# Optimization experiments

Measured on AMD Instinct MI355X. Metric: run time of the kernel, lower is better.

## Reference

```python
import jax, jax.numpy as jnp
import numpy as np

B, L, D = 2048, 64, 512


def setup_inputs() -> dict:
    key = jax.random.key(0)
    ks = jax.random.split(key, 20)
    s = 1.0 / np.sqrt(D)
    inp = {
        "query_entity_encoding": jax.random.normal(ks[0], (B, L, D), jnp.float32),
        "relation_encoding": jax.random.normal(ks[1], (B, D), jnp.float32),
        "mask_emb": jax.random.normal(ks[2], (1, D), jnp.float32),
        "pos_e": jax.random.normal(ks[3], (100, D), jnp.float32),
        "pos_r": jax.random.normal(ks[4], (100, D), jnp.float32),
        "We_q": jax.random.normal(ks[5], (D, D), jnp.float32) * s,
        "be_q": jnp.zeros((D,), jnp.float32),
        "We_k": jax.random.normal(ks[6], (D, D), jnp.float32) * s,
        "be_k": jnp.zeros((D,), jnp.float32),
        "We_v": jax.random.normal(ks[7], (D, D), jnp.float32) * s,
        "be_v": jnp.zeros((D,), jnp.float32),
        "Wr_q": jax.random.normal(ks[8], (D, D), jnp.float32) * s,
        "br_q": jnp.zeros((D,), jnp.float32),
        "Wr_k": jax.random.normal(ks[9], (D, D), jnp.float32) * s,
        "br_k": jnp.zeros((D,), jnp.float32),
        "Wr_v": jax.random.normal(ks[10], (D, D), jnp.float32) * s,
        "br_v": jnp.zeros((D,), jnp.float32),
    }
    return inp


def _linear(x, W, b):
    # torch nn.Linear: y = x @ W.T + b
    return jnp.einsum("bld,ed->ble", x, W) + b


def reference(query_entity_encoding, relation_encoding, mask_emb, pos_e, pos_r,
              We_q, be_q, We_k, be_k, We_v, be_v,
              Wr_q, br_q, Wr_k, br_k, Wr_v, br_v):
    b, l, d = query_entity_encoding.shape  # l <= 99 assumed (matches init spec)
    # append mask token, add positional encodings
    mask_tok = jnp.broadcast_to(mask_emb[None, :, :], (b, 1, d))
    ent = jnp.concatenate([query_entity_encoding, mask_tok], axis=1)  # [b, l+1, d]
    ent = ent + pos_e[: l + 1][None, :, :]
    rel = relation_encoding[:, None, :] + pos_r[:l][None, :, :]  # [b, l, d]
    # six projections
    Qe, Ke, Ve = _linear(ent, We_q, be_q), _linear(ent, We_k, be_k), _linear(ent, We_v, be_v)
    Qr, Kr, Vr = _linear(rel, Wr_q, br_q), _linear(rel, Wr_k, br_k), _linear(rel, Wr_v, br_v)
    # block-concat attention == attention over concatenated streams
    Q = jnp.concatenate([Qe, Qr], axis=1)  # [b, 2l+1, d]
    K = jnp.concatenate([Ke, Kr], axis=1)
    V = jnp.concatenate([Ve, Vr], axis=1)
    scale = 1.0 / jnp.sqrt(jnp.asarray(d, Q.dtype))
    A = jnp.einsum("bqd,bkd->bqk", Q, K) * scale
    A = jax.nn.softmax(A, axis=-1)
    out = jnp.einsum("bqk,bkd->bqd", A, V)
    return out[:, 0]
```

## Files before the change

kernel.cpp:

```cpp
#include <hip/hip_runtime.h>
#include <math.h>


using s16x8 = __attribute__((ext_vector_type(8))) short;
using f32x4 = __attribute__((ext_vector_type(4))) float;

#define S12 1216

static __device__ __forceinline__ float bf2f(unsigned short s) {
  union { unsigned u; float f; } c; c.u = ((unsigned)s) << 16; return c.f;
}
static __device__ __forceinline__ unsigned short f2bf(float f) {
  union { float f; unsigned u; } c; c.f = f;
  unsigned u = c.u;
  unsigned r = (u + 0x7fffu + ((u >> 16) & 1u)) >> 16;
  return (unsigned short)r;
}

template <int K>
__device__ __forceinline__ void mfma64(
    const unsigned short* __restrict__ Ab, int lda,
    const unsigned short* __restrict__ Bb, int ldb,
    int wm, int wn, int lr, int koff, f32x4 acc[2][2]) {
#pragma unroll
  for (int k0 = 0; k0 < K; k0 += 32) {
    s16x8 a[2], b[2];
#pragma unroll
    for (int im = 0; im < 2; ++im)
      a[im] = *(const s16x8*)(Ab + (size_t)(wm + im * 16 + lr) * lda + k0 + koff);
#pragma unroll
    for (int in = 0; in < 2; ++in)
      b[in] = *(const s16x8*)(Bb + (size_t)(wn + in * 16 + lr) * ldb + k0 + koff);
#pragma unroll
    for (int im = 0; im < 2; ++im)
#pragma unroll
      for (int in = 0; in < 2; ++in)
        acc[im][in] = __builtin_amdgcn_mfma_f32_16x16x32_bf16(a[im], b[in], acc[im][in], 0, 0, 0);
  }
}

__global__ __launch_bounds__(256) void prep_kernel(
    const float* __restrict__ x, const float* __restrict__ rel,
    const float* __restrict__ pos_e, const float* __restrict__ pos_r,
    const float* __restrict__ maskv, const float* __restrict__ We_q,
    const float* __restrict__ We_k, const float* __restrict__ Wr_k,
    const float* __restrict__ We_v, const float* __restrict__ Wr_v,
    const float* __restrict__ be_k, const float* __restrict__ br_k,
    unsigned short* __restrict__ Xp, unsigned short* __restrict__ relb,
    unsigned short* __restrict__ Weqb, unsigned short* __restrict__ Wkb,
    unsigned short* __restrict__ WekT, unsigned short* __restrict__ Bt,
    unsigned short* __restrict__ Paug) {
  const int blk = blockIdx.x, tid = threadIdx.x;
  __shared__ float ts[64][65];
  if (blk < 2048) {
    float2 v = *(const float2*)(x + (size_t)blk * 32768 + tid * 2);
    float2 pe = *(const float2*)(pos_e + tid * 2);
    ushort2 o;
    o.x = f2bf(v.x + pe.x);
    o.y = f2bf(v.y + pe.y);
    *(ushort2*)(Xp + (size_t)blk * 512 + tid * 2) = o;
    float2 rv = *(const float2*)(rel + (size_t)blk * 512 + tid * 2);
    ushort2 ro;
    ro.x = f2bf(rv.x);
    ro.y = f2bf(rv.y);
    *(ushort2*)(relb + (size_t)blk * 512 + tid * 2) = ro;
  } else if (blk < 2176) {
    const int e = ((blk - 2048) * 256 + tid) * 8;
    float4 a0 = *(const float4*)(We_q + e);
    float4 a1 = *(const float4*)(We_q + e + 4);
    ushort4 o0, o1;
    o0.x = f2bf(a0.x); o0.y = f2bf(a0.y); o0.z = f2bf(a0.z); o0.w = f2bf(a0.w);
    o1.x = f2bf(a1.x); o1.y = f2bf(a1.y); o1.z = f2bf(a1.z); o1.w = f2bf(a1.w);
    *(ushort4*)(Weqb + e) = o0;
    *(ushort4*)(Weqb + e + 4) = o1;
  } else if (blk < 2432) {
    const int e = ((blk - 2176) * 256 + tid) * 8;
    const int n = e >> 10, k = e & 1023;
    const float* src = (k < 512) ? (We_k + (size_t)n * 512 + k)
                                 : (Wr_k + (size_t)n * 512 + k - 512);
    float4 v0 = *(const float4*)src;
    float4 v1 = *(const float4*)(src + 4);
    ushort4 o0, o1;
    o0.x = f2bf(v0.x); o0.y = f2bf(v0.y); o0.z = f2bf(v0.z); o0.w = f2bf(v0.w);
    o1.x = f2bf(v1.x); o1.y = f2bf(v1.y); o1.z = f2bf(v1.z); o1.w = f2bf(v1.w);
    *(ushort4*)(Wkb + e) = o0;
    *(ushort4*)(Wkb + e + 4) = o1;
  } else if (blk < 2496) {
    const int tr = blk - 2432;
    const int td0 = (tr >> 3) * 64, tn0 = (tr & 7) * 64;
    const int r = tid >> 2, cq = (tid & 3) * 16;
#pragma unroll
    for (int i = 0; i < 16; i += 4) {
      float4 v = *(const float4*)(We_k + (size_t)(tn0 + r) * 512 + td0 + cq + i);
      ts[r][cq + i + 0] = v.x;
      ts[r][cq + i + 1] = v.y;
      ts[r][cq + i + 2] = v.z;
      ts[r][cq + i + 3] = v.w;
    }
    __syncthreads();
#pragma unroll
    for (int i = 0; i < 16; i += 4) {
      ushort4 o;
      o.x = f2bf(ts[cq + i + 0][r]);
      o.y = f2bf(ts[cq + i + 1][r]);
      o.z = f2bf(ts[cq + i + 2][r]);
      o.w = f2bf(ts[cq + i + 3][r]);
      *(ushort4*)(WekT + (size_t)(td0 + r) * 512 + tn0 + cq + i) = o;
    }
  } else if (blk == 2496) {
    WekT[(size_t)512 * 512 + tid] = f2bf(be_k[tid]);
    WekT[(size_t)512 * 512 + 256 + tid] = f2bf(be_k[256 + tid]);
    WekT[(size_t)513 * 512 + tid] = f2bf(br_k[tid]);
    WekT[(size_t)513 * 512 + 256 + tid] = f2bf(br_k[256 + tid]);
  } else if (blk < 2513) {
    const int e = ((blk - 2497) * 256 + tid) * 8;
    if (e < 62 * 512) {
      ushort4 z = {0, 0, 0, 0};
      *(ushort4*)(WekT + (size_t)514 * 512 + e) = z;
      *(ushort4*)(WekT + (size_t)514 * 512 + e + 4) = z;
    }
  } else if (blk < 3025) {
    const int base = ((blk - 2513) * 256 + tid) * 4;
    const int n = base >> 10, k = base & 1023;
    const float* src = (k < 512) ? (We_v + (size_t)n * 512 + k)
                                 : (Wr_v + (size_t)n * 512 + k - 512);
    float4 v = *(const float4*)src;
    ushort4 o;
    o.x = f2bf(v.x); o.y = f2bf(v.y); o.z = f2bf(v.z); o.w = f2bf(v.w);
    *(ushort4*)(Bt + (size_t)n * S12 + k) = o;
  } else if (blk < 3041) {
    const int t = (blk - 3025) * 256 + tid;
    const int n = t >> 3, c0 = 1152 + (t & 7) * 8;
    ushort4 z = {0, 0, 0, 0};
    *(ushort4*)(Bt + (size_t)n * S12 + c0) = z;
    *(ushort4*)(Bt + (size_t)n * S12 + c0 + 4) = z;
  } else {
    const int idx = (blk - 3041) * 256 + tid;
    const int e = idx * 8;
    const int j = e >> 10, c = e & 1023;
    ushort4 o0 = {0, 0, 0, 0}, o1 = {0, 0, 0, 0};
    if (j < 65 && c < 512) {
      float4 v0 = *(const float4*)(pos_e + (size_t)j * 512 + c);
      float4 v1 = *(const float4*)(pos_e + (size_t)j * 512 + c + 4);
      if (j == 64) {
        float4 m0 = *(const float4*)(maskv + c);
        float4 m1 = *(const float4*)(maskv + c + 4);
        v0.x += m0.x; v0.y += m0.y; v0.z += m0.z; v0.w += m0.w;
        v1.x += m1.x; v1.y += m1.y; v1.z += m1.z; v1.w += m1.w;
      }
      o0.x = f2bf(v0.x); o0.y = f2bf(v0.y); o0.z = f2bf(v0.z); o0.w = f2bf(v0.w);
      o1.x = f2bf(v1.x); o1.y = f2bf(v1.y); o1.z = f2bf(v1.z); o1.w = f2bf(v1.w);
    } else if (j >= 65 && j < 129 && c >= 512) {
      float4 v0 = *(const float4*)(pos_r + (size_t)(j - 65) * 512 + c - 512);
      float4 v1 = *(const float4*)(pos_r + (size_t)(j - 65) * 512 + c - 512 + 4);
      o0.x = f2bf(v0.x); o0.y = f2bf(v0.y); o0.z = f2bf(v0.z); o0.w = f2bf(v0.w);
      o1.x = f2bf(v1.x); o1.y = f2bf(v1.y); o1.z = f2bf(v1.z); o1.w = f2bf(v1.w);
    }
    *(ushort4*)(Paug + e) = o0;
    *(ushort4*)(Paug + e + 4) = o1;
  }
}

__global__ __launch_bounds__(256) void g1_kernel(
    const unsigned short* __restrict__ Xp, const unsigned short* __restrict__ Weqb,
    const float* __restrict__ be_q, const unsigned short* __restrict__ relb,
    const unsigned short* __restrict__ Wkb, const unsigned short* __restrict__ Paug,
    unsigned short* __restrict__ Bt, unsigned short* __restrict__ qb,
    float* __restrict__ RW, unsigned short* __restrict__ GP) {
  int blk = blockIdx.x;
  const int tid = threadIdx.x;
  const int wid = tid >> 6, lane = tid & 63;
  const int wm = (wid >> 1) * 32, wn = (wid & 1) * 32;
  const int lr = lane & 15, koff = (lane >> 4) * 8;
  const int r0 = (lane >> 4) * 4;
  f32x4 acc[2][2] = {};
  if (blk < 256) {
    const int bm = (blk >> 3) * 64, bn = (blk & 7) * 64;
    mfma64<512>(Xp + (size_t)bm * 512, 512, Weqb + (size_t)bn * 512, 512,
                wm, wn, lr, koff, acc);
#pragma unroll
    for (int im = 0; im < 2; ++im)
#pragma unroll
      for (int in = 0; in < 2; ++in)
#pragma unroll
        for (int i = 0; i < 4; ++i) {
          const int row = bm + wm + im * 16 + r0 + i;
          const int col = bn + wn + in * 16 + lr;
          qb[(size_t)row * 512 + col] = f2bf(acc[im][in][i] + be_q[col]);
        }
  } else if (blk < 512) {
    blk -= 256;
    const int bm = (blk >> 3) * 64, bn = (blk & 7) * 64;
    mfma64<512>(relb + (size_t)bm * 512, 512, Wkb + (size_t)bn * 1024 + 512, 1024,
                wm, wn, lr, koff, acc);
#pragma unroll
    for (int im = 0; im < 2; ++im)
#pragma unroll
      for (int in = 0; in < 2; ++in)
#pragma unroll
        for (int i = 0; i < 4; ++i) {
          const int row = bm + wm + im * 16 + r0 + i;
          const int col = bn + wn + in * 16 + lr;
          RW[(size_t)row * 512 + col] = acc[im][in][i];
        }
  } else if (blk < 536) {
    blk -= 512;
    const int bm = (blk >> 3) * 64, bn = (blk & 7) * 64;
    mfma64<1024>(Paug + (size_t)bm * 1024, 1024, Wkb + (size_t)bn * 1024, 1024,
                 wm, wn, lr, koff, acc);
#pragma unroll
    for (int im = 0; im < 2; ++im)
#pragma unroll
      for (int in = 0; in < 2; ++in)
#pragma unroll
        for (int i = 0; i < 4; ++i) {
          const int row = bm + wm + im * 16 + r0 + i;
          const int col = bn + wn + in * 16 + lr;
          GP[(size_t)row * 512 + col] = f2bf(acc[im][in][i]);
        }
  } else {
    blk -= 536;
    const int bm = (blk >> 3) * 64, bn = (blk & 7) * 64;
    mfma64<1024>(Paug + (size_t)bm * 1024, 1024, Bt + (size_t)bn * S12, S12,
                 wm, wn, lr, koff, acc);
#pragma unroll
    for (int im = 0; im < 2; ++im)
#pragma unroll
      for (int in = 0; in < 2; ++in)
#pragma unroll
        for (int i = 0; i < 4; ++i) {
          const int row = bm + wm + im * 16 + r0 + i;
          const int col = bn + wn + in * 16 + lr;
          if (row < 129)
            Bt[(size_t)col * S12 + 1024 + row] = f2bf(acc[im][in][i]);
        }
  }
}

__global__ __launch_bounds__(256) void g2_kernel(
    const unsigned short* __restrict__ qb, const unsigned short* __restrict__ WekT,
    const unsigned short* __restrict__ GP, float* __restrict__ qke,
    float* __restrict__ sd) {
  int blk = blockIdx.x;
  const int tid = threadIdx.x;
  const int wid = tid >> 6, lane = tid & 63;
  const int wm = (wid >> 1) * 32, wn = (wid & 1) * 32;
  const int lr = lane & 15, koff = (lane >> 4) * 8;
  const int r0 = (lane >> 4) * 4;
  f32x4 acc[2][2] = {};
  if (blk < 288) {
    const int bm = (blk / 9) * 64, bn = (blk % 9) * 64;
    mfma64<512>(qb + (size_t)bm * 512, 512, WekT + (size_t)bn * 512, 512,
                wm, wn, lr, koff, acc);
#pragma unroll
    for (int im = 0; im < 2; ++im)
#pragma unroll
      for (int in = 0; in < 2; ++in)
#pragma unroll
        for (int i = 0; i < 4; ++i) {
          const int row = bm + wm + im * 16 + r0 + i;
          const int col = bn + wn + in * 16 + lr;
          qke[(size_t)row * 576 + col] = acc[im][in][i];
        }
  } else {
    blk -= 288;
    const int bm = (blk / 3) * 64, bn = (blk % 3) * 64;
    mfma64<512>(qb + (size_t)bm * 512, 512, GP + (size_t)bn * 512, 512,
                wm, wn, lr, koff, acc);
#pragma unroll
    for (int im = 0; im < 2; ++im)
#pragma unroll
      for (int in = 0; in < 2; ++in)
#pragma unroll
        for (int i = 0; i < 4; ++i) {
          const int row = bm + wm + im * 16 + r0 + i;
          const int col = bn + wn + in * 16 + lr;
          sd[(size_t)row * 192 + col] = acc[im][in][i];
        }
  }
}

__global__ __launch_bounds__(512, 4) void attn_kernel(
    const float* __restrict__ x, const float* __restrict__ rel,
    const float* __restrict__ qke, const float* __restrict__ sd,
    const unsigned short* __restrict__ qb, const float* __restrict__ RW,
    unsigned short* __restrict__ A, float* __restrict__ spe_g,
    float* __restrict__ spr_g) {
  __shared__ unsigned short xs[64 * 512];
  __shared__ unsigned short part[8 * 512];
  __shared__ float sdl[192];
  __shared__ float sc[64];
  __shared__ float pvv[129];
  __shared__ float scx[8];
  const int b = blockIdx.x;
  const int tid = threadIdx.x;
  const int wid = tid >> 6, lane = tid & 63;
  const int j0 = wid * 8;
  const float scale = 0.04419417382415922f;
  const float* xb = x + (size_t)b * 32768;

  if (tid < 192) sdl[tid] = sd[(size_t)b * 192 + tid];
  if (tid == 200) scx[1] = qke[(size_t)b * 576 + 512];
  float qe[8];
  {
    float4 a0 = *(const float4*)(qke + (size_t)b * 576 + lane * 8);
    float4 a1 = *(const float4*)(qke + (size_t)b * 576 + lane * 8 + 4);
    qe[0] = a0.x; qe[1] = a0.y; qe[2] = a0.z; qe[3] = a0.w;
    qe[4] = a1.x; qe[5] = a1.y; qe[6] = a1.z; qe[7] = a1.w;
  }

  {
    float a8[8];
#pragma unroll
    for (int c = 0; c < 2; ++c) {
      float4 w0[4], w1[4];
#pragma unroll
      for (int r = 0; r < 4; ++r) {
        const int j = j0 + c * 4 + r;
        w0[r] = *(const float4*)(xb + (size_t)j * 512 + lane * 8);
        w1[r] = *(const float4*)(xb + (size_t)j * 512 + lane * 8 + 4);
      }
#pragma unroll
      for (int r = 0; r < 4; ++r) {
        const int j = j0 + c * 4 + r;
        s16x8 u;
        u[0] = (short)f2bf(w0[r].x); u[1] = (short)f2bf(w0[r].y);
        u[2] = (short)f2bf(w0[r].z); u[3] = (short)f2bf(w0[r].w);
        u[4] = (short)f2bf(w1[r].x); u[5] = (short)f2bf(w1[r].y);
        u[6] = (short)f2bf(w1[r].z); u[7] = (short)f2bf(w1[r].w);
        *(s16x8*)(xs + (size_t)j * 512 + lane * 8) = u;
        a8[c * 4 + r] =
            qe[0] * w0[r].x + qe[1] * w0[r].y + qe[2] * w0[r].z + qe[3] * w0[r].w +
            qe[4] * w1[r].x + qe[5] * w1[r].y + qe[6] * w1[r].z + qe[7] * w1[r].w;
      }
    }
#pragma unroll
    for (int off = 32; off > 0; off >>= 1) {
#pragma unroll
      for (int r = 0; r < 8; ++r) a8[r] += __shfl_xor(a8[r], off);
    }
    if (lane == 0) {
#pragma unroll
      for (int r = 0; r < 8; ++r) sc[j0 + r] = a8[r];
    }
  }
  if (wid == 7) {
    s16x8 qv = *(const s16x8*)(qb + (size_t)b * 512 + lane * 8);
    float4 r0 = *(const float4*)(RW + (size_t)b * 512 + lane * 8);
    float4 r1 = *(const float4*)(RW + (size_t)b * 512 + lane * 8 + 4);
    float s = bf2f(qv[0]) * r0.x + bf2f(qv[1]) * r0.y + bf2f(qv[2]) * r0.z +
              bf2f(qv[3]) * r0.w + bf2f(qv[4]) * r1.x + bf2f(qv[5]) * r1.y +
              bf2f(qv[6]) * r1.z + bf2f(qv[7]) * r1.w;
#pragma unroll
    for (int off = 32; off > 0; off >>= 1) s += __shfl_xor(s, off);
    if (lane == 0) scx[0] = s + qke[(size_t)b * 576 + 513];
  }
  __syncthreads();

  if (wid == 0) {
    const float crr = scx[0];
    const float qbk = scx[1];
    float v1 = (sc[lane] + sdl[lane] + qbk) * scale;
    float v2 = (lane == 0) ? (sdl[64] + qbk) * scale : (sdl[64 + lane] + crr) * scale;
    float v3 = (lane == 0) ? (sdl[128] + crr) * scale : -1e30f;
    float m = fmaxf(fmaxf(v1, v2), v3);
#pragma unroll
    for (int off = 32; off > 0; off >>= 1) m = fmaxf(m, __shfl_xor(m, off));
    float e1 = __expf(v1 - m);
    float e2 = __expf(v2 - m);
    float e3 = (lane == 0) ? __expf(v3 - m) : 0.f;
    float se = e1 + ((lane == 0) ? e2 : 0.f);
    float sr = ((lane == 0) ? 0.f : e2) + e3;
#pragma unroll
    for (int off = 32; off > 0; off >>= 1) {
      se += __shfl_xor(se, off);
      sr += __shfl_xor(sr, off);
    }
    float inv = 1.f / (se + sr);
    float p1 = e1 * inv, p2 = e2 * inv;
    pvv[lane] = p1;
    pvv[64 + lane] = p2;
    unsigned short* Ab = A + (size_t)b * S12;
    Ab[1024 + lane] = f2bf(p1);
    Ab[1088 + lane] = f2bf(p2);
    if (lane == 0) {
      float p3 = e3 * inv;
      pvv[128] = p3;
      Ab[1152] = f2bf(p3);
      scx[4] = sr * inv;
      spe_g[b] = se * inv;
      spr_g[b] = sr * inv;
    } else {
      Ab[1152 + lane] = 0;
    }
  }
  __syncthreads();

  {
    float acc8[8] = {};
#pragma unroll
    for (int r = 0; r < 8; ++r) {
      const float p = pvv[j0 + r];
      s16x8 xv = *(const s16x8*)(xs + (size_t)(j0 + r) * 512 + lane * 8);
      acc8[0] += p * bf2f(xv[0]); acc8[1] += p * bf2f(xv[1]);
      acc8[2] += p * bf2f(xv[2]); acc8[3] += p * bf2f(xv[3]);
      acc8[4] += p * bf2f(xv[4]); acc8[5] += p * bf2f(xv[5]);
      acc8[6] += p * bf2f(xv[6]); acc8[7] += p * bf2f(xv[7]);
    }
    s16x8 o;
#pragma unroll
    for (int i = 0; i < 8; ++i) o[i] = (short)f2bf(acc8[i]);
    *(s16x8*)(part + wid * 512 + lane * 8) = o;
  }
  __syncthreads();
  {
    float s = 0.f;
#pragma unroll
    for (int w = 0; w < 8; ++w) s += bf2f(part[w * 512 + tid]);
    unsigned short* Ab = A + (size_t)b * S12;
    Ab[tid] = f2bf(s);
    Ab[512 + tid] = f2bf(scx[4] * rel[(size_t)b * 512 + tid]);
  }
}

__global__ __launch_bounds__(256) void out_mfma_kernel(
    const unsigned short* __restrict__ A, const unsigned short* __restrict__ Bt,
    const float* __restrict__ be_v, const float* __restrict__ br_v,
    const float* __restrict__ spe, const float* __restrict__ spr,
    float* __restrict__ outp) {
  const int bn = blockIdx.x * 64;
  const int bm = blockIdx.y * 64;
  const int tid = threadIdx.x;
  const int wid = tid >> 6, lane = tid & 63;
  const int wm = (wid >> 1) * 32, wn = (wid & 1) * 32;
  const int lr = lane & 15, koff = (lane >> 4) * 8;
  f32x4 acc[2][2] = {};
  mfma64<S12>(A + (size_t)bm * S12, S12, Bt + (size_t)bn * S12, S12,
              wm, wn, lr, koff, acc);
  const int r0 = (lane >> 4) * 4;
#pragma unroll
  for (int im = 0; im < 2; ++im)
#pragma unroll
    for (int i = 0; i < 4; ++i) {
      const int row = bm + wm + im * 16 + r0 + i;
      const float se = spe[row], sr = spr[row];
#pragma unroll
      for (int in = 0; in < 2; ++in) {
        const int col = bn + wn + in * 16 + lr;
        outp[(size_t)row * 512 + col] = acc[im][in][i] + se * be_v[col] + sr * br_v[col];
      }
    }
}

extern "C" void kernel_launch(void* const* d_in, const int* in_sizes, int n_in,
                              void* d_out, int out_size, void* d_ws, size_t ws_size,
                              hipStream_t stream) {
  const float* x     = (const float*)d_in[0];
  const float* rel   = (const float*)d_in[1];
  const float* maskv = (const float*)d_in[2];
  const float* pos_e = (const float*)d_in[3];
  const float* pos_r = (const float*)d_in[4];
  const float* We_q  = (const float*)d_in[5];
  const float* be_q  = (const float*)d_in[6];
  const float* We_k  = (const float*)d_in[7];
  const float* be_k  = (const float*)d_in[8];
  const float* We_v  = (const float*)d_in[9];
  const float* be_v  = (const float*)d_in[10];
  const float* Wr_k  = (const float*)d_in[13];
  const float* br_k  = (const float*)d_in[14];
  const float* Wr_v  = (const float*)d_in[15];
  const float* br_v  = (const float*)d_in[16];

  char* p = (char*)d_ws;
  float* qke = (float*)p;                     p += (size_t)2048 * 576 * 4;
  float* sd  = (float*)p;                     p += (size_t)2048 * 192 * 4;
  float* RW  = (float*)p;                     p += (size_t)2048 * 512 * 4;
  float* spe = (float*)p;                     p += 2048 * 4;
  float* spr = (float*)p;                     p += 2048 * 4;
  unsigned short* qb   = (unsigned short*)p;  p += (size_t)2048 * 512 * 2;
  unsigned short* A    = (unsigned short*)p;  p += (size_t)2048 * S12 * 2;
  unsigned short* Bt   = (unsigned short*)p;  p += (size_t)512 * S12 * 2;
  unsigned short* WekT = (unsigned short*)p;  p += (size_t)576 * 512 * 2;
  unsigned short* Weqb = (unsigned short*)p;  p += (size_t)512 * 512 * 2;
  unsigned short* Wkb  = (unsigned short*)p;  p += (size_t)512 * 1024 * 2;
  unsigned short* GP   = (unsigned short*)p;  p += (size_t)192 * 512 * 2;
  unsigned short* Paug = (unsigned short*)p;  p += (size_t)192 * 1024 * 2;
  unsigned short* Xp   = (unsigned short*)p;  p += (size_t)2048 * 512 * 2;
  unsigned short* relb = (unsigned short*)p;  p += (size_t)2048 * 512 * 2;
  float* outp = (float*)d_out;

  prep_kernel<<<3137, 256, 0, stream>>>(x, rel, pos_e, pos_r, maskv, We_q,
                                        We_k, Wr_k, We_v, Wr_v, be_k, br_k,
                                        Xp, relb, Weqb, Wkb, WekT, Bt, Paug);
  g1_kernel<<<560, 256, 0, stream>>>(Xp, Weqb, be_q, relb, Wkb, Paug, Bt, qb,
                                     RW, GP);
  g2_kernel<<<384, 256, 0, stream>>>(qb, WekT, GP, qke, sd);
  attn_kernel<<<2048, 512, 0, stream>>>(x, rel, qke, sd, qb, RW, A, spe, spr);
  out_mfma_kernel<<<dim3(8, 32), 256, 0, stream>>>(A, Bt, be_v, br_v, spe, spr,
                                                   outp);
}
```

Before: 130.4 us.

## Fuse activation bf16 conversion into GEMMs, store intermediates as bf16, split-K output GEMM

```diff
diff --git a/kernel.cpp b/kernel.cpp
--- a/kernel.cpp
+++ b/kernel.cpp
@@ -40,32 +40,18 @@
 }
 
 __global__ __launch_bounds__(256) void prep_kernel(
-    const float* __restrict__ x, const float* __restrict__ rel,
     const float* __restrict__ pos_e, const float* __restrict__ pos_r,
     const float* __restrict__ maskv, const float* __restrict__ We_q,
     const float* __restrict__ We_k, const float* __restrict__ Wr_k,
     const float* __restrict__ We_v, const float* __restrict__ Wr_v,
     const float* __restrict__ be_k, const float* __restrict__ br_k,
-    unsigned short* __restrict__ Xp, unsigned short* __restrict__ relb,
     unsigned short* __restrict__ Weqb, unsigned short* __restrict__ Wkb,
     unsigned short* __restrict__ WekT, unsigned short* __restrict__ Bt,
     unsigned short* __restrict__ Paug) {
   const int blk = blockIdx.x, tid = threadIdx.x;
   __shared__ float ts[64][65];
-  if (blk < 2048) {
-    float2 v = *(const float2*)(x + (size_t)blk * 32768 + tid * 2);
-    float2 pe = *(const float2*)(pos_e + tid * 2);
-    ushort2 o;
-    o.x = f2bf(v.x + pe.x);
-    o.y = f2bf(v.y + pe.y);
-    *(ushort2*)(Xp + (size_t)blk * 512 + tid * 2) = o;
-    float2 rv = *(const float2*)(rel + (size_t)blk * 512 + tid * 2);
-    ushort2 ro;
-    ro.x = f2bf(rv.x);
-    ro.y = f2bf(rv.y);
-    *(ushort2*)(relb + (size_t)blk * 512 + tid * 2) = ro;
-  } else if (blk < 2176) {
-    const int e = ((blk - 2048) * 256 + tid) * 8;
+  if (blk < 128) {
+    const int e = (blk * 256 + tid) * 8;
     float4 a0 = *(const float4*)(We_q + e);
     float4 a1 = *(const float4*)(We_q + e + 4);
     ushort4 o0, o1;
@@ -73,8 +59,8 @@
     o1.x = f2bf(a1.x); o1.y = f2bf(a1.y); o1.z = f2bf(a1.z); o1.w = f2bf(a1.w);
     *(ushort4*)(Weqb + e) = o0;
     *(ushort4*)(Weqb + e + 4) = o1;
-  } else if (blk < 2432) {
-    const int e = ((blk - 2176) * 256 + tid) * 8;
+  } else if (blk < 384) {
+    const int e = ((blk - 128) * 256 + tid) * 8;
     const int n = e >> 10, k = e & 1023;
     const float* src = (k < 512) ? (We_k + (size_t)n * 512 + k)
                                  : (Wr_k + (size_t)n * 512 + k - 512);
@@ -85,8 +71,8 @@
     o1.x = f2bf(v1.x); o1.y = f2bf(v1.y); o1.z = f2bf(v1.z); o1.w = f2bf(v1.w);
     *(ushort4*)(Wkb + e) = o0;
     *(ushort4*)(Wkb + e + 4) = o1;
-  } else if (blk < 2496) {
-    const int tr = blk - 2432;
+  } else if (blk < 448) {
+    const int tr = blk - 384;
     const int td0 = (tr >> 3) * 64, tn0 = (tr & 7) * 64;
     const int r = tid >> 2, cq = (tid & 3) * 16;
 #pragma unroll
@@ -107,20 +93,20 @@
       o.w = f2bf(ts[cq + i + 3][r]);
       *(ushort4*)(WekT + (size_t)(td0 + r) * 512 + tn0 + cq + i) = o;
     }
-  } else if (blk == 2496) {
+  } else if (blk == 448) {
     WekT[(size_t)512 * 512 + tid] = f2bf(be_k[tid]);
     WekT[(size_t)512 * 512 + 256 + tid] = f2bf(be_k[256 + tid]);
     WekT[(size_t)513 * 512 + tid] = f2bf(br_k[tid]);
     WekT[(size_t)513 * 512 + 256 + tid] = f2bf(br_k[256 + tid]);
-  } else if (blk < 2513) {
-    const int e = ((blk - 2497) * 256 + tid) * 8;
+  } else if (blk < 465) {
+    const int e = ((blk - 449) * 256 + tid) * 8;
     if (e < 62 * 512) {
       ushort4 z = {0, 0, 0, 0};
       *(ushort4*)(WekT + (size_t)514 * 512 + e) = z;
       *(ushort4*)(WekT + (size_t)514 * 512 + e + 4) = z;
     }
-  } else if (blk < 3025) {
-    const int base = ((blk - 2513) * 256 + tid) * 4;
+  } else if (blk < 977) {
+    const int base = ((blk - 465) * 256 + tid) * 4;
     const int n = base >> 10, k = base & 1023;
     const float* src = (k < 512) ? (We_v + (size_t)n * 512 + k)
                                  : (Wr_v + (size_t)n * 512 + k - 512);
@@ -128,14 +114,14 @@
     ushort4 o;
     o.x = f2bf(v.x); o.y = f2bf(v.y); o.z = f2bf(v.z); o.w = f2bf(v.w);
     *(ushort4*)(Bt + (size_t)n * S12 + k) = o;
-  } else if (blk < 3041) {
-    const int t = (blk - 3025) * 256 + tid;
+  } else if (blk < 993) {
+    const int t = (blk - 977) * 256 + tid;
     const int n = t >> 3, c0 = 1152 + (t & 7) * 8;
     ushort4 z = {0, 0, 0, 0};
     *(ushort4*)(Bt + (size_t)n * S12 + c0) = z;
     *(ushort4*)(Bt + (size_t)n * S12 + c0 + 4) = z;
   } else {
-    const int idx = (blk - 3041) * 256 + tid;
+    const int idx = (blk - 993) * 256 + tid;
     const int e = idx * 8;
     const int j = e >> 10, c = e & 1023;
     ushort4 o0 = {0, 0, 0, 0}, o1 = {0, 0, 0, 0};
@@ -162,11 +148,12 @@
 }
 
 __global__ __launch_bounds__(256) void g1_kernel(
-    const unsigned short* __restrict__ Xp, const unsigned short* __restrict__ Weqb,
-    const float* __restrict__ be_q, const unsigned short* __restrict__ relb,
-    const unsigned short* __restrict__ Wkb, const unsigned short* __restrict__ Paug,
-    unsigned short* __restrict__ Bt, unsigned short* __restrict__ qb,
-    float* __restrict__ RW, unsigned short* __restrict__ GP) {
+    const float* __restrict__ x, const float* __restrict__ pos_e,
+    const float* __restrict__ rel, const unsigned short* __restrict__ Weqb,
+    const float* __restrict__ be_q, const unsigned short* __restrict__ Wkb,
+    const unsigned short* __restrict__ Paug, unsigned short* __restrict__ Bt,
+    unsigned short* __restrict__ qb, float* __restrict__ RW,
+    unsigned short* __restrict__ GP) {
   int blk = blockIdx.x;
   const int tid = threadIdx.x;
   const int wid = tid >> 6, lane = tid & 63;
@@ -176,8 +163,32 @@
   f32x4 acc[2][2] = {};
   if (blk < 256) {
     const int bm = (blk >> 3) * 64, bn = (blk & 7) * 64;
-    mfma64<512>(Xp + (size_t)bm * 512, 512, Weqb + (size_t)bn * 512, 512,
-                wm, wn, lr, koff, acc);
+#pragma unroll
+    for (int k0 = 0; k0 < 512; k0 += 32) {
+      float4 p0 = *(const float4*)(pos_e + k0 + koff);
+      float4 p1 = *(const float4*)(pos_e + k0 + koff + 4);
+      s16x8 a[2], b[2];
+#pragma unroll
+      for (int im = 0; im < 2; ++im) {
+        const float* xr = x + (size_t)(bm + wm + im * 16 + lr) * 32768 + k0 + koff;
+        float4 v0 = *(const float4*)xr;
+        float4 v1 = *(const float4*)(xr + 4);
+        s16x8 u;
+        u[0] = (short)f2bf(v0.x + p0.x); u[1] = (short)f2bf(v0.y + p0.y);
+        u[2] = (short)f2bf(v0.z + p0.z); u[3] = (short)f2bf(v0.w + p0.w);
+        u[4] = (short)f2bf(v1.x + p1.x); u[5] = (short)f2bf(v1.y + p1.y);
+        u[6] = (short)f2bf(v1.z + p1.z); u[7] = (short)f2bf(v1.w + p1.w);
+        a[im] = u;
+      }
+#pragma unroll
+      for (int in = 0; in < 2; ++in)
+        b[in] = *(const s16x8*)(Weqb + (size_t)(bn + wn + in * 16 + lr) * 512 + k0 + koff);
+#pragma unroll
+      for (int im = 0; im < 2; ++im)
+#pragma unroll
+        for (int in = 0; in < 2; ++in)
+          acc[im][in] = __builtin_amdgcn_mfma_f32_16x16x32_bf16(a[im], b[in], acc[im][in], 0, 0, 0);
+    }
 #pragma unroll
     for (int im = 0; im < 2; ++im)
 #pragma unroll
@@ -191,8 +202,30 @@
   } else if (blk < 512) {
     blk -= 256;
     const int bm = (blk >> 3) * 64, bn = (blk & 7) * 64;
-    mfma64<512>(relb + (size_t)bm * 512, 512, Wkb + (size_t)bn * 1024 + 512, 1024,
-                wm, wn, lr, koff, acc);
+#pragma unroll
+    for (int k0 = 0; k0 < 512; k0 += 32) {
+      s16x8 a[2], b[2];
+#pragma unroll
+      for (int im = 0; im < 2; ++im) {
+        const float* rr = rel + (size_t)(bm + wm + im * 16 + lr) * 512 + k0 + koff;
+        float4 v0 = *(const float4*)rr;
+        float4 v1 = *(const float4*)(rr + 4);
+        s16x8 u;
+        u[0] = (short)f2bf(v0.x); u[1] = (short)f2bf(v0.y);
+        u[2] = (short)f2bf(v0.z); u[3] = (short)f2bf(v0.w);
+        u[4] = (short)f2bf(v1.x); u[5] = (short)f2bf(v1.y);
+        u[6] = (short)f2bf(v1.z); u[7] = (short)f2bf(v1.w);
+        a[im] = u;
+      }
+#pragma unroll
+      for (int in = 0; in < 2; ++in)
+        b[in] = *(const s16x8*)(Wkb + (size_t)(bn + wn + in * 16 + lr) * 1024 + 512 + k0 + koff);
+#pragma unroll
+      for (int im = 0; im < 2; ++im)
+#pragma unroll
+        for (int in = 0; in < 2; ++in)
+          acc[im][in] = __builtin_amdgcn_mfma_f32_16x16x32_bf16(a[im], b[in], acc[im][in], 0, 0, 0);
+    }
 #pragma unroll
     for (int im = 0; im < 2; ++im)
 #pragma unroll
@@ -216,7 +249,8 @@
         for (int i = 0; i < 4; ++i) {
           const int row = bm + wm + im * 16 + r0 + i;
           const int col = bn + wn + in * 16 + lr;
-          GP[(size_t)row * 512 + col] = f2bf(acc[im][in][i]);
+          if (row < 129)
+            GP[(size_t)row * 512 + col] = f2bf(acc[im][in][i]);
         }
   } else {
     blk -= 536;
@@ -239,8 +273,8 @@
 
 __global__ __launch_bounds__(256) void g2_kernel(
     const unsigned short* __restrict__ qb, const unsigned short* __restrict__ WekT,
-    const unsigned short* __restrict__ GP, float* __restrict__ qke,
-    float* __restrict__ sd) {
+    const unsigned short* __restrict__ GP, unsigned short* __restrict__ qkeb,
+    unsigned short* __restrict__ sdb) {
   int blk = blockIdx.x;
   const int tid = threadIdx.x;
   const int wid = tid >> 6, lane = tid & 63;
@@ -260,7 +294,7 @@
         for (int i = 0; i < 4; ++i) {
           const int row = bm + wm + im * 16 + r0 + i;
           const int col = bn + wn + in * 16 + lr;
-          qke[(size_t)row * 576 + col] = acc[im][in][i];
+          qkeb[(size_t)row * 576 + col] = f2bf(acc[im][in][i]);
         }
   } else {
     blk -= 288;
@@ -275,14 +309,14 @@
         for (int i = 0; i < 4; ++i) {
           const int row = bm + wm + im * 16 + r0 + i;
           const int col = bn + wn + in * 16 + lr;
-          sd[(size_t)row * 192 + col] = acc[im][in][i];
+          sdb[(size_t)row * 192 + col] = f2bf(acc[im][in][i]);
         }
   }
 }
 
 __global__ __launch_bounds__(512, 4) void attn_kernel(
     const float* __restrict__ x, const float* __restrict__ rel,
-    const float* __restrict__ qke, const float* __restrict__ sd,
+    const unsigned short* __restrict__ qkeb, const unsigned short* __restrict__ sdb,
     const unsigned short* __restrict__ qb, const float* __restrict__ RW,
     unsigned short* __restrict__ A, float* __restrict__ spe_g,
     float* __restrict__ spr_g) {
@@ -299,14 +333,14 @@
   const float scale = 0.04419417382415922f;
   const float* xb = x + (size_t)b * 32768;
 
-  if (tid < 192) sdl[tid] = sd[(size_t)b * 192 + tid];
-  if (tid == 200) scx[1] = qke[(size_t)b * 576 + 512];
+  const float relv = rel[(size_t)b * 512 + tid];
+  if (tid < 192) sdl[tid] = bf2f(sdb[(size_t)b * 192 + tid]);
+  if (tid == 200) scx[1] = bf2f(qkeb[(size_t)b * 576 + 512]);
   float qe[8];
   {
-    float4 a0 = *(const float4*)(qke + (size_t)b * 576 + lane * 8);
-    float4 a1 = *(const float4*)(qke + (size_t)b * 576 + lane * 8 + 4);
-    qe[0] = a0.x; qe[1] = a0.y; qe[2] = a0.z; qe[3] = a0.w;
-    qe[4] = a1.x; qe[5] = a1.y; qe[6] = a1.z; qe[7] = a1.w;
+    s16x8 qv = *(const s16x8*)(qkeb + (size_t)b * 576 + lane * 8);
+#pragma unroll
+    for (int i = 0; i < 8; ++i) qe[i] = bf2f(qv[i]);
   }
 
   {
@@ -353,7 +387,7 @@
               bf2f(qv[6]) * r1.z + bf2f(qv[7]) * r1.w;
 #pragma unroll
     for (int off = 32; off > 0; off >>= 1) s += __shfl_xor(s, off);
-    if (lane == 0) scx[0] = s + qke[(size_t)b * 576 + 513];
+    if (lane == 0) scx[0] = s + bf2f(qkeb[(size_t)b * 576 + 513]);
   }
   __syncthreads();
 
@@ -419,37 +453,52 @@
     for (int w = 0; w < 8; ++w) s += bf2f(part[w * 512 + tid]);
     unsigned short* Ab = A + (size_t)b * S12;
     Ab[tid] = f2bf(s);
-    Ab[512 + tid] = f2bf(scx[4] * rel[(size_t)b * 512 + tid]);
-  }
-}
-
-__global__ __launch_bounds__(256) void out_mfma_kernel(
+    Ab[512 + tid] = f2bf(scx[4] * relv);
+  }
+}
+
+__global__ __launch_bounds__(512) void out_mfma_kernel(
     const unsigned short* __restrict__ A, const unsigned short* __restrict__ Bt,
     const float* __restrict__ be_v, const float* __restrict__ br_v,
     const float* __restrict__ spe, const float* __restrict__ spr,
     float* __restrict__ outp) {
+  __shared__ float red[64][65];
   const int bn = blockIdx.x * 64;
   const int bm = blockIdx.y * 64;
   const int tid = threadIdx.x;
   const int wid = tid >> 6, lane = tid & 63;
-  const int wm = (wid >> 1) * 32, wn = (wid & 1) * 32;
+  const int grp = wid >> 2, w4 = wid & 3;
+  const int wm = (w4 >> 1) * 32, wn = (w4 & 1) * 32;
   const int lr = lane & 15, koff = (lane >> 4) * 8;
+  const int r0 = (lane >> 4) * 4;
   f32x4 acc[2][2] = {};
-  mfma64<S12>(A + (size_t)bm * S12, S12, Bt + (size_t)bn * S12, S12,
-              wm, wn, lr, koff, acc);
-  const int r0 = (lane >> 4) * 4;
-#pragma unroll
-  for (int im = 0; im < 2; ++im)
-#pragma unroll
-    for (int i = 0; i < 4; ++i) {
-      const int row = bm + wm + im * 16 + r0 + i;
-      const float se = spe[row], sr = spr[row];
-#pragma unroll
-      for (int in = 0; in < 2; ++in) {
-        const int col = bn + wn + in * 16 + lr;
-        outp[(size_t)row * 512 + col] = acc[im][in][i] + se * be_v[col] + sr * br_v[col];
+  mfma64<608>(A + (size_t)bm * S12 + grp * 608, S12,
+              Bt + (size_t)bn * S12 + grp * 608, S12, wm, wn, lr, koff, acc);
+  if (grp == 1) {
+#pragma unroll
+    for (int im = 0; im < 2; ++im)
+#pragma unroll
+      for (int in = 0; in < 2; ++in)
+#pragma unroll
+        for (int i = 0; i < 4; ++i)
+          red[wm + im * 16 + r0 + i][wn + in * 16 + lr] = acc[im][in][i];
+  }
+  __syncthreads();
+  if (grp == 0) {
+#pragma unroll
+    for (int im = 0; im < 2; ++im)
+#pragma unroll
+      for (int i = 0; i < 4; ++i) {
+        const int row = bm + wm + im * 16 + r0 + i;
+        const float se = spe[row], sr = spr[row];
+#pragma unroll
+        for (int in = 0; in < 2; ++in) {
+          const int col = bn + wn + in * 16 + lr;
+          const float v = acc[im][in][i] + red[wm + im * 16 + r0 + i][wn + in * 16 + lr];
+          outp[(size_t)row * 512 + col] = v + se * be_v[col] + sr * br_v[col];
+        }
       }
-    }
+  }
 }
 
 extern "C" void kernel_launch(void* const* d_in, const int* in_sizes, int n_in,
@@ -472,8 +521,6 @@
   const float* br_v  = (const float*)d_in[16];
 
   char* p = (char*)d_ws;
-  float* qke = (float*)p;                     p += (size_t)2048 * 576 * 4;
-  float* sd  = (float*)p;                     p += (size_t)2048 * 192 * 4;
   float* RW  = (float*)p;                     p += (size_t)2048 * 512 * 4;
   float* spe = (float*)p;                     p += 2048 * 4;
   float* spr = (float*)p;                     p += 2048 * 4;
@@ -485,17 +532,17 @@
   unsigned short* Wkb  = (unsigned short*)p;  p += (size_t)512 * 1024 * 2;
   unsigned short* GP   = (unsigned short*)p;  p += (size_t)192 * 512 * 2;
   unsigned short* Paug = (unsigned short*)p;  p += (size_t)192 * 1024 * 2;
-  unsigned short* Xp   = (unsigned short*)p;  p += (size_t)2048 * 512 * 2;
-  unsigned short* relb = (unsigned short*)p;  p += (size_t)2048 * 512 * 2;
+  unsigned short* qkeb = (unsigned short*)p;  p += (size_t)2048 * 576 * 2;
+  unsigned short* sdb  = (unsigned short*)p;  p += (size_t)2048 * 192 * 2;
   float* outp = (float*)d_out;
 
-  prep_kernel<<<3137, 256, 0, stream>>>(x, rel, pos_e, pos_r, maskv, We_q,
-                                        We_k, Wr_k, We_v, Wr_v, be_k, br_k,
-                                        Xp, relb, Weqb, Wkb, WekT, Bt, Paug);
-  g1_kernel<<<560, 256, 0, stream>>>(Xp, Weqb, be_q, relb, Wkb, Paug, Bt, qb,
-                                     RW, GP);
-  g2_kernel<<<384, 256, 0, stream>>>(qb, WekT, GP, qke, sd);
-  attn_kernel<<<2048, 512, 0, stream>>>(x, rel, qke, sd, qb, RW, A, spe, spr);
-  out_mfma_kernel<<<dim3(8, 32), 256, 0, stream>>>(A, Bt, be_v, br_v, spe, spr,
+  prep_kernel<<<1089, 256, 0, stream>>>(pos_e, pos_r, maskv, We_q, We_k, Wr_k,
+                                        We_v, Wr_v, be_k, br_k, Weqb, Wkb,
+                                        WekT, Bt, Paug);
+  g1_kernel<<<560, 256, 0, stream>>>(x, pos_e, rel, Weqb, be_q, Wkb, Paug, Bt,
+                                     qb, RW, GP);
+  g2_kernel<<<384, 256, 0, stream>>>(qb, WekT, GP, qkeb, sdb);
+  attn_kernel<<<2048, 512, 0, stream>>>(x, rel, qkeb, sdb, qb, RW, A, spe, spr);
+  out_mfma_kernel<<<dim3(8, 32), 512, 0, stream>>>(A, Bt, be_v, br_v, spe, spr,
                                                    outp);
 }
```

New measurement: 139.1 us. 6.6% more time.

## Merge prep, g1 and g2 kernels into one persistent kernel with grid barriers

Applied to the files above, without the earlier changes.

```diff
diff --git a/kernel.cpp b/kernel.cpp
--- a/kernel.cpp
+++ b/kernel.cpp
@@ -6,6 +6,7 @@
 using f32x4 = __attribute__((ext_vector_type(4))) float;
 
 #define S12 1216
+#define PREGRID 512
 
 static __device__ __forceinline__ float bf2f(unsigned short s) {
   union { unsigned u; float f; } c; c.u = ((unsigned)s) << 16; return c.f;
@@ -39,59 +40,68 @@
   }
 }
 
-__global__ __launch_bounds__(256) void prep_kernel(
-    const float* __restrict__ x, const float* __restrict__ rel,
-    const float* __restrict__ pos_e, const float* __restrict__ pos_r,
-    const float* __restrict__ maskv, const float* __restrict__ We_q,
-    const float* __restrict__ We_k, const float* __restrict__ Wr_k,
-    const float* __restrict__ We_v, const float* __restrict__ Wr_v,
-    const float* __restrict__ be_k, const float* __restrict__ br_k,
-    unsigned short* __restrict__ Xp, unsigned short* __restrict__ relb,
-    unsigned short* __restrict__ Weqb, unsigned short* __restrict__ Wkb,
-    unsigned short* __restrict__ WekT, unsigned short* __restrict__ Bt,
-    unsigned short* __restrict__ Paug) {
-  const int blk = blockIdx.x, tid = threadIdx.x;
+struct PreParams {
+  const float *x, *rel, *pos_e, *pos_r, *maskv;
+  const float *We_q, *We_k, *Wr_k, *We_v, *Wr_v, *be_k, *br_k, *be_q;
+  unsigned short *Xp, *relb, *Weqb, *Wkb, *WekT, *Bt, *Paug, *qb, *GP;
+  float *RW, *qke, *sd;
+  unsigned* bar;
+};
+
+static __device__ __forceinline__ void gbar(unsigned* c) {
+  __syncthreads();
+  __threadfence();
+  if (threadIdx.x == 0) {
+    atomicAdd(c, 1u);
+    while (atomicAdd(c, 0u) < (unsigned)PREGRID) __builtin_amdgcn_s_sleep(16);
+  }
+  __syncthreads();
+  __threadfence();
+}
+
+static __device__ void prep_work(int blk, const PreParams& P) {
+  const int tid = threadIdx.x;
   __shared__ float ts[64][65];
   if (blk < 2048) {
-    float2 v = *(const float2*)(x + (size_t)blk * 32768 + tid * 2);
-    float2 pe = *(const float2*)(pos_e + tid * 2);
+    float2 v = *(const float2*)(P.x + (size_t)blk * 32768 + tid * 2);
+    float2 pe = *(const float2*)(P.pos_e + tid * 2);
     ushort2 o;
     o.x = f2bf(v.x + pe.x);
     o.y = f2bf(v.y + pe.y);
-    *(ushort2*)(Xp + (size_t)blk * 512 + tid * 2) = o;
-    float2 rv = *(const float2*)(rel + (size_t)blk * 512 + tid * 2);
+    *(ushort2*)(P.Xp + (size_t)blk * 512 + tid * 2) = o;
+    float2 rv = *(const float2*)(P.rel + (size_t)blk * 512 + tid * 2);
     ushort2 ro;
     ro.x = f2bf(rv.x);
     ro.y = f2bf(rv.y);
-    *(ushort2*)(relb + (size_t)blk * 512 + tid * 2) = ro;
+    *(ushort2*)(P.relb + (size_t)blk * 512 + tid * 2) = ro;
   } else if (blk < 2176) {
     const int e = ((blk - 2048) * 256 + tid) * 8;
-    float4 a0 = *(const float4*)(We_q + e);
-    float4 a1 = *(const float4*)(We_q + e + 4);
+    float4 a0 = *(const float4*)(P.We_q + e);
+    float4 a1 = *(const float4*)(P.We_q + e + 4);
     ushort4 o0, o1;
     o0.x = f2bf(a0.x); o0.y = f2bf(a0.y); o0.z = f2bf(a0.z); o0.w = f2bf(a0.w);
     o1.x = f2bf(a1.x); o1.y = f2bf(a1.y); o1.z = f2bf(a1.z); o1.w = f2bf(a1.w);
-    *(ushort4*)(Weqb + e) = o0;
-    *(ushort4*)(Weqb + e + 4) = o1;
+    *(ushort4*)(P.Weqb + e) = o0;
+    *(ushort4*)(P.Weqb + e + 4) = o1;
   } else if (blk < 2432) {
     const int e = ((blk - 2176) * 256 + tid) * 8;
     const int n = e >> 10, k = e & 1023;
-    const float* src = (k < 512) ? (We_k + (size_t)n * 512 + k)
-                                 : (Wr_k + (size_t)n * 512 + k - 512);
+    const float* src = (k < 512) ? (P.We_k + (size_t)n * 512 + k)
+                                 : (P.Wr_k + (size_t)n * 512 + k - 512);
     float4 v0 = *(const float4*)src;
     float4 v1 = *(const float4*)(src + 4);
     ushort4 o0, o1;
     o0.x = f2bf(v0.x); o0.y = f2bf(v0.y); o0.z = f2bf(v0.z); o0.w = f2bf(v0.w);
     o1.x = f2bf(v1.x); o1.y = f2bf(v1.y); o1.z = f2bf(v1.z); o1.w = f2bf(v1.w);
-    *(ushort4*)(Wkb + e) = o0;
-    *(ushort4*)(Wkb + e + 4) = o1;
+    *(ushort4*)(P.Wkb + e) = o0;
+    *(ushort4*)(P.Wkb + e + 4) = o1;
   } else if (blk < 2496) {
     const int tr = blk - 2432;
     const int td0 = (tr >> 3) * 64, tn0 = (tr & 7) * 64;
     const int r = tid >> 2, cq = (tid & 3) * 16;
 #pragma unroll
     for (int i = 0; i < 16; i += 4) {
-      float4 v = *(const float4*)(We_k + (size_t)(tn0 + r) * 512 + td0 + cq + i);
+      float4 v = *(const float4*)(P.We_k + (size_t)(tn0 + r) * 512 + td0 + cq + i);
       ts[r][cq + i + 0] = v.x;
       ts[r][cq + i + 1] = v.y;
       ts[r][cq + i + 2] = v.z;
@@ -105,69 +115,64 @@
       o.y = f2bf(ts[cq + i + 1][r]);
       o.z = f2bf(ts[cq + i + 2][r]);
       o.w = f2bf(ts[cq + i + 3][r]);
-      *(ushort4*)(WekT + (size_t)(td0 + r) * 512 + tn0 + cq + i) = o;
-    }
+      *(ushort4*)(P.WekT + (size_t)(td0 + r) * 512 + tn0 + cq + i) = o;
+    }
+    __syncthreads();
   } else if (blk == 2496) {
-    WekT[(size_t)512 * 512 + tid] = f2bf(be_k[tid]);
-    WekT[(size_t)512 * 512 + 256 + tid] = f2bf(be_k[256 + tid]);
-    WekT[(size_t)513 * 512 + tid] = f2bf(br_k[tid]);
-    WekT[(size_t)513 * 512 + 256 + tid] = f2bf(br_k[256 + tid]);
+    P.WekT[(size_t)512 * 512 + tid] = f2bf(P.be_k[tid]);
+    P.WekT[(size_t)512 * 512 + 256 + tid] = f2bf(P.be_k[256 + tid]);
+    P.WekT[(size_t)513 * 512 + tid] = f2bf(P.br_k[tid]);
+    P.WekT[(size_t)513 * 512 + 256 + tid] = f2bf(P.br_k[256 + tid]);
   } else if (blk < 2513) {
     const int e = ((blk - 2497) * 256 + tid) * 8;
     if (e < 62 * 512) {
       ushort4 z = {0, 0, 0, 0};
-      *(ushort4*)(WekT + (size_t)514 * 512 + e) = z;
-      *(ushort4*)(WekT + (size_t)514 * 512 + e + 4) = z;
+      *(ushort4*)(P.WekT + (size_t)514 * 512 + e) = z;
+      *(ushort4*)(P.WekT + (size_t)514 * 512 + e + 4) = z;
     }
   } else if (blk < 3025) {
     const int base = ((blk - 2513) * 256 + tid) * 4;
     const int n = base >> 10, k = base & 1023;
-    const float* src = (k < 512) ? (We_v + (size_t)n * 512 + k)
-                                 : (Wr_v + (size_t)n * 512 + k - 512);
+    const float* src = (k < 512) ? (P.We_v + (size_t)n * 512 + k)
+                                 : (P.Wr_v + (size_t)n * 512 + k - 512);
     float4 v = *(const float4*)src;
     ushort4 o;
     o.x = f2bf(v.x); o.y = f2bf(v.y); o.z = f2bf(v.z); o.w = f2bf(v.w);
-    *(ushort4*)(Bt + (size_t)n * S12 + k) = o;
+    *(ushort4*)(P.Bt + (size_t)n * S12 + k) = o;
   } else if (blk < 3041) {
     const int t = (blk - 3025) * 256 + tid;
     const int n = t >> 3, c0 = 1152 + (t & 7) * 8;
     ushort4 z = {0, 0, 0, 0};
-    *(ushort4*)(Bt + (size_t)n * S12 + c0) = z;
-    *(ushort4*)(Bt + (size_t)n * S12 + c0 + 4) = z;
+    *(ushort4*)(P.Bt + (size_t)n * S12 + c0) = z;
+    *(ushort4*)(P.Bt + (size_t)n * S12 + c0 + 4) = z;
   } else {
     const int idx = (blk - 3041) * 256 + tid;
     const int e = idx * 8;
     const int j = e >> 10, c = e & 1023;
     ushort4 o0 = {0, 0, 0, 0}, o1 = {0, 0, 0, 0};
     if (j < 65 && c < 512) {
-      float4 v0 = *(const float4*)(pos_e + (size_t)j * 512 + c);
-      float4 v1 = *(const float4*)(pos_e + (size_t)j * 512 + c + 4);
+      float4 v0 = *(const float4*)(P.pos_e + (size_t)j * 512 + c);
+      float4 v1 = *(const float4*)(P.pos_e + (size_t)j * 512 + c + 4);
       if (j == 64) {
-        float4 m0 = *(const float4*)(maskv + c);
-        float4 m1 = *(const float4*)(maskv + c + 4);
+        float4 m0 = *(const float4*)(P.maskv + c);
+        float4 m1 = *(const float4*)(P.maskv + c + 4);
         v0.x += m0.x; v0.y += m0.y; v0.z += m0.z; v0.w += m0.w;
         v1.x += m1.x; v1.y += m1.y; v1.z += m1.z; v1.w += m1.w;
       }
       o0.x = f2bf(v0.x); o0.y = f2bf(v0.y); o0.z = f2bf(v0.z); o0.w = f2bf(v0.w);
       o1.x = f2bf(v1.x); o1.y = f2bf(v1.y); o1.z = f2bf(v1.z); o1.w = f2bf(v1.w);
     } else if (j >= 65 && j < 129 && c >= 512) {
-      float4 v0 = *(const float4*)(pos_r + (size_t)(j - 65) * 512 + c - 512);
-      float4 v1 = *(const float4*)(pos_r + (size_t)(j - 65) * 512 + c - 512 + 4);
+      float4 v0 = *(const float4*)(P.pos_r + (size_t)(j - 65) * 512 + c - 512);
+      float4 v1 = *(const float4*)(P.pos_r + (size_t)(j - 65) * 512 + c - 512 + 4);
       o0.x = f2bf(v0.x); o0.y = f2bf(v0.y); o0.z = f2bf(v0.z); o0.w = f2bf(v0.w);
       o1.x = f2bf(v1.x); o1.y = f2bf(v1.y); o1.z = f2bf(v1.z); o1.w = f2bf(v1.w);
     }
-    *(ushort4*)(Paug + e) = o0;
-    *(ushort4*)(Paug + e + 4) = o1;
-  }
-}
-
-__global__ __launch_bounds__(256) void g1_kernel(
-    const unsigned short* __restrict__ Xp, const unsigned short* __restrict__ Weqb,
-    const float* __restrict__ be_q, const unsigned short* __restrict__ relb,
-    const unsigned short* __restrict__ Wkb, const unsigned short* __restrict__ Paug,
-    unsigned short* __restrict__ Bt, unsigned short* __restrict__ qb,
-    float* __restrict__ RW, unsigned short* __restrict__ GP) {
-  int blk = blockIdx.x;
+    *(ushort4*)(P.Paug + e) = o0;
+    *(ushort4*)(P.Paug + e + 4) = o1;
+  }
+}
+
+static __device__ void g1_work(int blk, const PreParams& P) {
   const int tid = threadIdx.x;
   const int wid = tid >> 6, lane = tid & 63;
   const int wm = (wid >> 1) * 32, wn = (wid & 1) * 32;
@@ -176,7 +181,7 @@
   f32x4 acc[2][2] = {};
   if (blk < 256) {
     const int bm = (blk >> 3) * 64, bn = (blk & 7) * 64;
-    mfma64<512>(Xp + (size_t)bm * 512, 512, Weqb + (size_t)bn * 512, 512,
+    mfma64<512>(P.Xp + (size_t)bm * 512, 512, P.Weqb + (size_t)bn * 512, 512,
                 wm, wn, lr, koff, acc);
 #pragma unroll
     for (int im = 0; im < 2; ++im)
@@ -186,12 +191,12 @@
         for (int i = 0; i < 4; ++i) {
           const int row = bm + wm + im * 16 + r0 + i;
           const int col = bn + wn + in * 16 + lr;
-          qb[(size_t)row * 512 + col] = f2bf(acc[im][in][i] + be_q[col]);
+          P.qb[(size_t)row * 512 + col] = f2bf(acc[im][in][i] + P.be_q[col]);
         }
   } else if (blk < 512) {
     blk -= 256;
     const int bm = (blk >> 3) * 64, bn = (blk & 7) * 64;
-    mfma64<512>(relb + (size_t)bm * 512, 512, Wkb + (size_t)bn * 1024 + 512, 1024,
+    mfma64<512>(P.relb + (size_t)bm * 512, 512, P.Wkb + (size_t)bn * 1024 + 512, 1024,
                 wm, wn, lr, koff, acc);
 #pragma unroll
     for (int im = 0; im < 2; ++im)
@@ -201,12 +206,12 @@
         for (int i = 0; i < 4; ++i) {
           const int row = bm + wm + im * 16 + r0 + i;
           const int col = bn + wn + in * 16 + lr;
-          RW[(size_t)row * 512 + col] = acc[im][in][i];
+          P.RW[(size_t)row * 512 + col] = acc[im][in][i];
         }
   } else if (blk < 536) {
     blk -= 512;
     const int bm = (blk >> 3) * 64, bn = (blk & 7) * 64;
-    mfma64<1024>(Paug + (size_t)bm * 1024, 1024, Wkb + (size_t)bn * 1024, 1024,
+    mfma64<1024>(P.Paug + (size_t)bm * 1024, 1024, P.Wkb + (size_t)bn * 1024, 1024,
                  wm, wn, lr, koff, acc);
 #pragma unroll
     for (int im = 0; im < 2; ++im)
@@ -216,12 +221,12 @@
         for (int i = 0; i < 4; ++i) {
           const int row = bm + wm + im * 16 + r0 + i;
           const int col = bn + wn + in * 16 + lr;
-          GP[(size_t)row * 512 + col] = f2bf(acc[im][in][i]);
+          P.GP[(size_t)row * 512 + col] = f2bf(acc[im][in][i]);
         }
   } else {
     blk -= 536;
     const int bm = (blk >> 3) * 64, bn = (blk & 7) * 64;
-    mfma64<1024>(Paug + (size_t)bm * 1024, 1024, Bt + (size_t)bn * S12, S12,
+    mfma64<1024>(P.Paug + (size_t)bm * 1024, 1024, P.Bt + (size_t)bn * S12, S12,
                  wm, wn, lr, koff, acc);
 #pragma unroll
     for (int im = 0; im < 2; ++im)
@@ -232,16 +237,12 @@
           const int row = bm + wm + im * 16 + r0 + i;
           const int col = bn + wn + in * 16 + lr;
           if (row < 129)
-            Bt[(size_t)col * S12 + 1024 + row] = f2bf(acc[im][in][i]);
+            P.Bt[(size_t)col * S12 + 1024 + row] = f2bf(acc[im][in][i]);
         }
   }
 }
 
-__global__ __launch_bounds__(256) void g2_kernel(
-    const unsigned short* __restrict__ qb, const unsigned short* __restrict__ WekT,
-    const unsigned short* __restrict__ GP, float* __restrict__ qke,
-    float* __restrict__ sd) {
-  int blk = blockIdx.x;
+static __device__ void g2_work(int blk, const PreParams& P) {
   const int tid = threadIdx.x;
   const int wid = tid >> 6, lane = tid & 63;
   const int wm = (wid >> 1) * 32, wn = (wid & 1) * 32;
@@ -250,7 +251,7 @@
   f32x4 acc[2][2] = {};
   if (blk < 288) {
     const int bm = (blk / 9) * 64, bn = (blk % 9) * 64;
-    mfma64<512>(qb + (size_t)bm * 512, 512, WekT + (size_t)bn * 512, 512,
+    mfma64<512>(P.qb + (size_t)bm * 512, 512, P.WekT + (size_t)bn * 512, 512,
                 wm, wn, lr, koff, acc);
 #pragma unroll
     for (int im = 0; im < 2; ++im)
@@ -260,12 +261,12 @@
         for (int i = 0; i < 4; ++i) {
           const int row = bm + wm + im * 16 + r0 + i;
           const int col = bn + wn + in * 16 + lr;
-          qke[(size_t)row * 576 + col] = acc[im][in][i];
+          P.qke[(size_t)row * 576 + col] = acc[im][in][i];
         }
   } else {
     blk -= 288;
     const int bm = (blk / 3) * 64, bn = (blk % 3) * 64;
-    mfma64<512>(qb + (size_t)bm * 512, 512, GP + (size_t)bn * 512, 512,
+    mfma64<512>(P.qb + (size_t)bm * 512, 512, P.GP + (size_t)bn * 512, 512,
                 wm, wn, lr, koff, acc);
 #pragma unroll
     for (int im = 0; im < 2; ++im)
@@ -275,9 +276,17 @@
         for (int i = 0; i < 4; ++i) {
           const int row = bm + wm + im * 16 + r0 + i;
           const int col = bn + wn + in * 16 + lr;
-          sd[(size_t)row * 192 + col] = acc[im][in][i];
+          P.sd[(size_t)row * 192 + col] = acc[im][in][i];
         }
   }
+}
+
+__global__ __launch_bounds__(256, 2) void pre_kernel(PreParams P) {
+  for (int item = blockIdx.x; item < 3137; item += PREGRID) prep_work(item, P);
+  gbar(P.bar + 0);
+  for (int item = blockIdx.x; item < 560; item += PREGRID) g1_work(item, P);
+  gbar(P.bar + 32);
+  if (blockIdx.x < 384) g2_work(blockIdx.x, P);
 }
 
 __global__ __launch_bounds__(512, 4) void attn_kernel(
@@ -487,14 +496,19 @@
   unsigned short* Paug = (unsigned short*)p;  p += (size_t)192 * 1024 * 2;
   unsigned short* Xp   = (unsigned short*)p;  p += (size_t)2048 * 512 * 2;
   unsigned short* relb = (unsigned short*)p;  p += (size_t)2048 * 512 * 2;
+  unsigned* bar = (unsigned*)p;               p += 256;
   float* outp = (float*)d_out;
 
-  prep_kernel<<<3137, 256, 0, stream>>>(x, rel, pos_e, pos_r, maskv, We_q,
-                                        We_k, Wr_k, We_v, Wr_v, be_k, br_k,
-                                        Xp, relb, Weqb, Wkb, WekT, Bt, Paug);
-  g1_kernel<<<560, 256, 0, stream>>>(Xp, Weqb, be_q, relb, Wkb, Paug, Bt, qb,
-                                     RW, GP);
-  g2_kernel<<<384, 256, 0, stream>>>(qb, WekT, GP, qke, sd);
+  PreParams P;
+  P.x = x; P.rel = rel; P.pos_e = pos_e; P.pos_r = pos_r; P.maskv = maskv;
+  P.We_q = We_q; P.We_k = We_k; P.Wr_k = Wr_k; P.We_v = We_v; P.Wr_v = Wr_v;
+  P.be_k = be_k; P.br_k = br_k; P.be_q = be_q;
+  P.Xp = Xp; P.relb = relb; P.Weqb = Weqb; P.Wkb = Wkb; P.WekT = WekT;
+  P.Bt = Bt; P.Paug = Paug; P.qb = qb; P.GP = GP;
+  P.RW = RW; P.qke = qke; P.sd = sd; P.bar = bar;
+
+  hipMemsetAsync(bar, 0, 256, stream);
+  pre_kernel<<<PREGRID, 256, 0, stream>>>(P);
   attn_kernel<<<2048, 512, 0, stream>>>(x, rel, qke, sd, qb, RW, A, spe, spr);
   out_mfma_kernel<<<dim3(8, 32), 256, 0, stream>>>(A, Bt, be_v, br_v, spe, spr,
                                                    outp);
```

After: 339.5 us. +160.2%, slower.
